# Optimization experiments

Measured on AMD Instinct MI355X. Metric: run time of the kernel, lower is better.

Reference implementation:

```python
import jax, jax.numpy as jnp
import numpy as np

B, D, H, E = 1024, 64, 128, 8192


def setup_inputs() -> dict:
    key = jax.random.key(0)
    ks = jax.random.split(key, 10)
    def w(k, shape, fan_in):
        return jax.random.normal(k, shape, jnp.float32) / np.float32(np.sqrt(fan_in))
    return {
        "mu": jax.random.normal(ks[0], (B, D), jnp.float32),
        "current_edge_index": jax.random.randint(ks[1], (2, E), 0, B),
        "W1": w(ks[2], (D, H), D),   "b1": jnp.zeros((H,), jnp.float32),
        "W2": w(ks[3], (H, H), H),   "b2": jnp.zeros((H,), jnp.float32),
        "Ws1": w(ks[4], (2 * H, H), 2 * H), "bs1": jnp.zeros((H,), jnp.float32),
        "Ws2": w(ks[5], (H, 1), H),  "bs2": jnp.zeros((1,), jnp.float32),
        "Wg1": w(ks[6], (2 * H, H), 2 * H), "bg1": jnp.zeros((H,), jnp.float32),
        "Wg2": w(ks[7], (H, D), H), "bg2": jnp.zeros((D,), jnp.float32),
    }


def _gcn(x, W, b, src, dst, n):
    loop = jnp.arange(n)
    s = jnp.concatenate([src, loop])
    d = jnp.concatenate([dst, loop])
    deg = jax.ops.segment_sum(jnp.ones_like(s, x.dtype), d, num_segments=n)
    dinv = jax.lax.rsqrt(jnp.maximum(deg, 1e-12))
    norm = dinv[s] * dinv[d]                      # [E+n]
    xw = x @ W                                    # [n,H]
    out = jax.ops.segment_sum(xw[s] * norm[:, None], d, num_segments=n)
    return out + b


def _pairwise_scores(h, Ws1, bs1, Ws2, bs2):
    # score_mlp([h_i || h_j]) for all pairs, vectorized: split first-layer weight
    A = h @ Ws1[:H]                               # [B,H] contribution of h_i
    C = h @ Ws1[H:]                               # [B,H] contribution of h_j
    pre = jax.nn.relu(A[:, None, :] + C[None, :, :] + bs1)   # [B,B,H]
    s = (pre @ Ws2)[..., 0] + bs2[0]              # [B,B]
    up = jnp.triu(s, 1)                           # only i<j computed in original
    return up + up.T                              # symmetric, zero diagonal


def _kruskal(scores_np, n):
    iu, ju = np.triu_indices(n, 1)
    w = scores_np[iu, ju]
    order = np.argsort(-w, kind="stable")         # descending, stable like list.sort
    parent = list(range(n))
    rank = [0] * n
    def find(u):
        while parent[u] != u:
            parent[u] = parent[parent[u]]
            u = parent[u]
        return u
    edges = []
    for k in order:
        i, j = int(iu[k]), int(ju[k])
        ri, rj = find(i), find(j)
        if ri == rj:
            continue
        if rank[ri] < rank[rj]:
            parent[ri] = rj
        elif rank[ri] > rank[rj]:
            parent[rj] = ri
        else:
            parent[rj] = ri
            rank[ri] += 1
        edges.append((i, j))
        if len(edges) == n - 1:
            break
    return np.asarray(edges, dtype=np.int64)      # [n-1, 2]


def reference(mu, current_edge_index, W1, b1, W2, b2, Ws1, bs1, Ws2, bs2, Wg1, bg1, Wg2, bg2):
    src, dst = current_edge_index[0], current_edge_index[1]
    h = jax.nn.relu(_gcn(mu, W1, b1, src, dst, B))
    h = jax.nn.relu(_gcn(h, W2, b2, src, dst, B))
    scores = _pairwise_scores(h, Ws1, bs1, Ws2, bs2)          # [B,B]
    mst = _kruskal(np.asarray(scores), B)                     # [B-1,2], i<j
    ei = jnp.asarray(mst[:, 0])
    ej = jnp.asarray(mst[:, 1])
    # bidirectional edge index: src=[i,j,...], dst=[j,i,...]
    new_edge_index = jnp.stack([
        jnp.stack([ei, ej], axis=1).reshape(-1),
        jnp.stack([ej, ei], axis=1).reshape(-1),
    ], axis=0)                                                # [2, 2*(B-1)]
    hp = jnp.concatenate([h[ei], h[ej]], axis=1)              # [B-1, 2H]
    gamma = jnp.tanh(jax.nn.relu(hp @ Wg1 + bg1) @ Wg2 + bg2) # [B-1, D]
    return (new_edge_index, gamma)
```

## Files before the change

kernel.cpp:

```cpp
#include <hip/hip_runtime.h>
#include <hip/hip_bf16.h>
#include <math.h>

#define BN 1024
#define DIN 64
#define HD 128
#define EN 8192
#define SLOTS_STRIDE 64
#define MMR 8
#define NC 128

typedef unsigned long long u64;

__global__ void k_fill(const int* dst, int* cnt, int* slots) {
    int e = blockIdx.x * blockDim.x + threadIdx.x;
    if (e < EN) {
        int d = dst[e];
        int p = atomicAdd(&cnt[d], 1);
        if (p < SLOTS_STRIDE) slots[d * SLOTS_STRIDE + p] = e;
    }
}

__global__ __launch_bounds__(128) void k_finish(int* slots, const int* cnt, float* dinv) {
    __shared__ int buf[128][65];
    int tid = threadIdx.x;
    int t = blockIdx.x * 128 + tid;
    int n = cnt[t];
    if (n > SLOTS_STRIDE) n = SLOTS_STRIDE;
    for (int k = 0; k < n; k++) buf[tid][k] = slots[t * SLOTS_STRIDE + k];
    for (int k = 1; k < n; k++) {
        int v = buf[tid][k];
        int q = k - 1;
        while (q >= 0 && buf[tid][q] > v) { buf[tid][q + 1] = buf[tid][q]; q--; }
        buf[tid][q + 1] = v;
    }
    for (int k = 0; k < n; k++) slots[t * SLOTS_STRIDE + k] = buf[tid][k];
    dinv[t] = 1.0f / sqrtf(fmaxf((float)(n + 1), 1e-12f));
}

__global__ __launch_bounds__(128) void k_mm8(const float* x, const float* W, const float* bias,
                                             float* out, int K) {
    __shared__ float xr[MMR][HD];
    int col = threadIdx.x;
    int r0 = blockIdx.x * MMR;
#pragma unroll
    for (int r = 0; r < MMR; r++)
        if (col < K) xr[r][col] = x[(r0 + r) * K + col];
    __syncthreads();
    float b = bias ? bias[col] : 0.0f;
    float acc[MMR];
#pragma unroll
    for (int r = 0; r < MMR; r++) acc[r] = b;
#pragma unroll 4
    for (int k = 0; k < K; k++) {
        float w = W[k * HD + col];
#pragma unroll
        for (int r = 0; r < MMR; r++) acc[r] = fmaf(xr[r][k], w, acc[r]);
    }
#pragma unroll
    for (int r = 0; r < MMR; r++) out[(r0 + r) * HD + col] = acc[r];
}

__global__ __launch_bounds__(128) void k_mmAC(const float* h, const float* Ws1, const float* bs1,
                                              float* Aa, float* Cc) {
    __shared__ float xr[MMR][HD];
    int col = threadIdx.x;
    int r0 = blockIdx.x * MMR;
#pragma unroll
    for (int r = 0; r < MMR; r++) xr[r][col] = h[(r0 + r) * HD + col];
    __syncthreads();
    float accA[MMR], accC[MMR];
    float bc = bs1[col];
#pragma unroll
    for (int r = 0; r < MMR; r++) { accA[r] = 0.0f; accC[r] = bc; }
#pragma unroll 2
    for (int k = 0; k < HD; k++) {
        float wa = Ws1[k * HD + col];
        float wc = Ws1[(HD + k) * HD + col];
#pragma unroll
        for (int r = 0; r < MMR; r++) {
            accA[r] = fmaf(xr[r][k], wa, accA[r]);
            accC[r] = fmaf(xr[r][k], wc, accC[r]);
        }
    }
#pragma unroll
    for (int r = 0; r < MMR; r++) {
        Aa[(r0 + r) * HD + col] = accA[r];
        Cc[(r0 + r) * HD + col] = accC[r];
    }
}

__global__ __launch_bounds__(128) void k_gather(const float* xw, const float* bvec, const int* src,
                                                const int* slots, const int* cnt,
                                                const float* dinv, float* hout) {
    int d = blockIdx.x, t = threadIdx.x;
    float dd = dinv[d];
    float acc = 0.0f;
    int base = d * SLOTS_STRIDE, n = cnt[d];
    if (n > SLOTS_STRIDE) n = SLOTS_STRIDE;
    for (int s = 0; s < n; s++) {
        int e = slots[base + s];
        int sn = src[e];
        acc = fmaf(xw[sn * HD + t], dinv[sn] * dd, acc);
    }
    acc = fmaf(xw[d * HD + t], dd * dd, acc);
    acc += bvec[t];
    hout[d * HD + t] = fmaxf(acc, 0.0f);
}

__device__ __forceinline__ u64 edge_key(float w, int i, int j) {
    unsigned u = __float_as_uint(w);
    u = (u & 0x80000000u) ? ~u : (u | 0x80000000u);
    int a = i < j ? i : j, b = i < j ? j : i;
    unsigned packed = (unsigned)(a * BN + b);
    return ((u64)u << 20) | (u64)(0xFFFFFu - packed);
}

__global__ __launch_bounds__(256) void k_scores(const float* Aa, const float* Cc,
                                                const float* Ws2, const float* bs2v,
                                                float* S, u64* best) {
    int bi = blockIdx.y, bj = blockIdx.x;
    if (bi > bj) return;
    __shared__ float As[64][68];
    __shared__ float Cs[64][68];
    __shared__ float w2[HD];
    __shared__ u64 rmax[64], cmax[64];
    int tid = threadIdx.x;
    int R = bi * 64, Cb = bj * 64;
    if (tid < HD) w2[tid] = Ws2[tid];
    if (tid < 64) { rmax[tid] = 0ull; cmax[tid] = 0ull; }
    int tx = tid & 15, ty = tid >> 4;
    float acc[4][4] = {};
    for (int half = 0; half < 2; half++) {
        int k0 = half * 64;
        __syncthreads();
        for (int idx = tid; idx < 64 * 64; idx += 256) {
            int row = idx >> 6;
            int kk = idx & 63;
            As[kk][row] = Aa[(R + row) * HD + k0 + kk];
            Cs[kk][row] = Cc[(Cb + row) * HD + k0 + kk];
        }
        __syncthreads();
        for (int kk = 0; kk < 64; kk++) {
            float4 av = *(const float4*)&As[kk][ty * 4];
            float4 cv = *(const float4*)&Cs[kk][tx * 4];
            float wk = w2[k0 + kk];
            float ar[4] = {av.x, av.y, av.z, av.w};
            float cr[4] = {cv.x, cv.y, cv.z, cv.w};
#pragma unroll
            for (int r = 0; r < 4; r++)
#pragma unroll
                for (int q = 0; q < 4; q++) {
                    float tv = fmaxf(ar[r] + cr[q], 0.0f);
                    acc[r][q] = fmaf(tv, wk, acc[r][q]);
                }
        }
    }
    float b2 = bs2v[0];
    u64 rloc[4] = {0ull, 0ull, 0ull, 0ull};
    u64 cloc[4] = {0ull, 0ull, 0ull, 0ull};
#pragma unroll
    for (int r = 0; r < 4; r++)
#pragma unroll
        for (int q = 0; q < 4; q++) {
            int gr = R + ty * 4 + r, gc = Cb + tx * 4 + q;
            float v = acc[r][q] + b2;
            if (gr < gc) {
                S[gr * BN + gc] = v;
                S[gc * BN + gr] = v;
                u64 key = edge_key(v, gr, gc);
                if (key > rloc[r]) rloc[r] = key;
                if (key > cloc[q]) cloc[q] = key;
            } else if (gr == gc) S[gr * BN + gc] = 0.0f;
        }
#pragma unroll
    for (int r = 0; r < 4; r++) {
        if (rloc[r]) atomicMax(&rmax[ty * 4 + r], rloc[r]);
        if (cloc[r]) atomicMax(&cmax[tx * 4 + r], cloc[r]);
    }
    __syncthreads();
    if (tid < 64) {
        if (rmax[tid]) atomicMax(&best[R + tid], rmax[tid]);
    } else if (tid < 128) {
        if (cmax[tid - 64]) atomicMax(&best[Cb + tid - 64], cmax[tid - 64]);
    }
}

__global__ __launch_bounds__(256) void k_best(const float* S, const int* comp,
                                              u64* best, const int* mstcnt) {
    if (*mstcnt >= BN - 1) return;
    int lane = threadIdx.x & 63;
    int i = blockIdx.x * 4 + (threadIdx.x >> 6);
    int ci = comp[i];
    const float* Srow = S + (size_t)i * BN;
    u64 loc = 0ull;
    for (int j = lane; j < BN; j += 64)
        if (comp[j] != ci) {
            u64 key = edge_key(Srow[j], i, j);
            if (key > loc) loc = key;
        }
#pragma unroll
    for (int off = 32; off > 0; off >>= 1) {
        u64 o = __shfl_xor(loc, off);
        if (o > loc) loc = o;
    }
    if (lane == 0 && loc) atomicMax(&best[ci], loc);
}

__global__ __launch_bounds__(1024) void k_merge1(u64* best, int* comp, u64* mst, int* mstcnt) {
    __shared__ int pa[BN], pb[BN];
    int c = threadIdx.x;
    u64 e = best[c];
    unsigned packed = 0xFFFFFu - (unsigned)(e & 0xFFFFFu);
    int a = packed >> 10, b = packed & 1023;
    int t = (a == c) ? b : a;
    pa[c] = t;
    __syncthreads();
    bool mutual = (pa[t] == c);
    int p0 = pa[c];
    if (mutual && c < t) p0 = c;
    __syncthreads();
    pa[c] = p0;
    __syncthreads();
    if (!(mutual && c > t)) {
        int idx = atomicAdd(mstcnt, 1);
        mst[idx] = e;
    }
    for (int it = 0; it < 10; it++) {
        pb[c] = pa[pa[c]];
        __syncthreads();
        pa[c] = pb[c];
        __syncthreads();
    }
    comp[c] = pa[c];
    best[c] = 0ull;
}

__global__ __launch_bounds__(1024) void k_merge(int* comp, u64* best, u64* mst, int* mstcnt,
                                                int* compD, int* ncompG, int emitDense) {
    __shared__ int pa[BN], pb[BN];
    int c = threadIdx.x;
    if (*mstcnt >= BN - 1) return;
    int myComp = comp[c];
    bool root = (myComp == c);
    u64 e = best[c];
    int t = c;
    if (root && e) {
        unsigned packed = 0xFFFFFu - (unsigned)(e & 0xFFFFFu);
        int a = packed >> 10, b = packed & 1023;
        int ca = comp[a], cb = comp[b];
        t = (ca == c) ? cb : ca;
    }
    pa[c] = (root && e) ? t : c;
    __syncthreads();
    bool mutual = root && e && (pa[t] == c);
    int p0 = pa[c];
    if (mutual && c < t) p0 = c;
    __syncthreads();
    pa[c] = p0;
    __syncthreads();
    if (root && e && !(mutual && c > t)) {
        int idx = atomicAdd(mstcnt, 1);
        mst[idx] = e;
    }
    for (int it = 0; it < 10; it++) {
        pb[c] = pa[pa[c]];
        __syncthreads();
        pa[c] = pb[c];
        __syncthreads();
    }
    comp[c] = pa[myComp];
    best[c] = 0ull;
    if (!emitDense) return;
    __syncthreads();
    int isR = (comp[c] == c) ? 1 : 0;
    pa[c] = isR;
    __syncthreads();
    for (int d = 1; d < BN; d <<= 1) {
        int v = (c >= d) ? pa[c - d] : 0;
        __syncthreads();
        pa[c] += v;
        __syncthreads();
    }
    if (isR) pb[c] = pa[c] - 1;
    __syncthreads();
    compD[c] = pb[comp[c]];
    if (c == BN - 1) *ncompG = pa[BN - 1];
}

__global__ __launch_bounds__(256) void k_Gsp(const float* S, const int* compD,
                                             const int* mstcnt, u64* spG) {
    if (*mstcnt >= BN - 1) return;
    __shared__ u64 t[NC];
    int tid = threadIdx.x;
    int i = blockIdx.x;
    int ci = compD[i];
    if (tid < NC) t[tid] = 0ull;
    __syncthreads();
    const float* Srow = S + (size_t)i * BN;
    for (int j = tid; j < BN; j += 256) {
        int cj = compD[j];
        if (j != i && cj != ci) atomicMax(&t[cj], edge_key(Srow[j], i, j));
    }
    __syncthreads();
    if (tid < NC && t[tid]) atomicMax(&spG[(size_t)ci * NC + tid], t[tid]);
}

struct FinSm {
    union {
        u64 sp[NC][NC];
        u64 sk[BN];
    } u;
    int cnd[BN];
    int ccomp[NC], cpa[NC], cpb[NC];
    u64 cbest[NC];
    int lcnt;
};

__global__ __launch_bounds__(1024) void k_mstfin(const u64* spG, const int* compD,
                                                 const int* ncompG, const int* mstcntG,
                                                 u64* mstG, float* out, int* pairs) {
    __shared__ FinSm sm;
    int c = threadIdx.x;
    int total = *mstcntG;
    if (total < BN - 1) {
        int nc = *ncompG;
        for (int idx = c; idx < NC * NC; idx += 1024) ((u64*)sm.u.sp)[idx] = spG[idx];
        sm.cnd[c] = compD[c];
        if (c < NC) { sm.ccomp[c] = c; sm.cbest[c] = 0ull; }
        if (c == 0) sm.lcnt = 0;
        __syncthreads();
        for (int rr = 0; rr < 8 && total < BN - 1; rr++) {
            if (c < nc) {
                int g = sm.ccomp[c];
                u64 m = 0ull;
                for (int c2 = 0; c2 < nc; c2++)
                    if (sm.ccomp[c2] != g) {
                        u64 v = sm.u.sp[c][c2];
                        if (v > m) m = v;
                    }
                if (m) atomicMax(&sm.cbest[g], m);
            }
            __syncthreads();
            if (c < nc) {
                bool root = (sm.ccomp[c] == c);
                u64 e = sm.cbest[c];
                int t2 = c;
                if (root && e) {
                    unsigned packed = 0xFFFFFu - (unsigned)(e & 0xFFFFFu);
                    int a = packed >> 10, b = packed & 1023;
                    int ga = sm.ccomp[sm.cnd[a]], gb = sm.ccomp[sm.cnd[b]];
                    t2 = (ga == c) ? gb : ga;
                }
                sm.cpa[c] = (root && e) ? t2 : c;
            }
            __syncthreads();
            if (c < nc) {
                bool root = (sm.ccomp[c] == c);
                u64 e = sm.cbest[c];
                int t2 = sm.cpa[c];
                bool mutual = root && e && (sm.cpa[t2] == c);
                int p0 = sm.cpa[c];
                if (mutual && c < t2) p0 = c;
                sm.cpb[c] = p0;
                if (root && e && !(mutual && c > t2)) {
                    int idx = total + atomicAdd(&sm.lcnt, 1);
                    mstG[idx] = e;
                }
            }
            __syncthreads();
            if (c < nc) sm.cpa[c] = sm.cpb[c];
            __syncthreads();
            for (int it = 0; it < 7; it++) {
                if (c < nc) sm.cpb[c] = sm.cpa[sm.cpa[c]];
                __syncthreads();
                if (c < nc) sm.cpa[c] = sm.cpb[c];
                __syncthreads();
            }
            if (c < nc) {
                sm.ccomp[c] = sm.cpa[sm.ccomp[c]];
                sm.cbest[c] = 0ull;
            }
            __syncthreads();
            int added = sm.lcnt;
            __syncthreads();
            total += added;
            if (c == 0) sm.lcnt = 0;
            __syncthreads();
        }
    }
    __syncthreads();
    sm.u.sk[c] = (c < BN - 1) ? mstG[c] : 0ull;
    __syncthreads();
    if (c < BN - 1) {
        u64 mykey = sm.u.sk[c];
        int rk = 0;
        for (int f = 0; f < BN - 1; f++) rk += (sm.u.sk[f] > mykey) ? 1 : 0;
        unsigned packed = 0xFFFFFu - (unsigned)(mykey & 0xFFFFFu);
        int i = packed >> 10, j2 = packed & 1023;
        out[2 * rk] = (float)i;
        out[2 * rk + 1] = (float)j2;
        out[2046 + 2 * rk] = (float)j2;
        out[2046 + 2 * rk + 1] = (float)i;
        pairs[2 * rk] = i;
        pairs[2 * rk + 1] = j2;
    }
}

__global__ __launch_bounds__(128) void k_gamma(const float* h, const int* pairs,
                                               const float* Wg1, const float* bg1,
                                               const float* Wg2, const float* bg2, float* out) {
    int eidx = blockIdx.x;
    __shared__ float hp[2 * HD];
    __shared__ float z1[HD];
    int t = threadIdx.x;
    int i = pairs[2 * eidx], j = pairs[2 * eidx + 1];
    hp[t] = h[i * HD + t];
    hp[HD + t] = h[j * HD + t];
    __syncthreads();
    float acc = bg1[t];
    for (int k = 0; k < 2 * HD; k++) acc = fmaf(hp[k], Wg1[k * HD + t], acc);
    z1[t] = fmaxf(acc, 0.0f);
    __syncthreads();
    if (t < DIN) {
        float g = bg2[t];
        for (int k = 0; k < HD; k++) g = fmaf(z1[k], Wg2[k * DIN + t], g);
        out[4092 + eidx * DIN + t] = tanhf(g);
    }
}

extern "C" void kernel_launch(void* const* d_in, const int* in_sizes, int n_in,
                              void* d_out, int out_size, void* d_ws, size_t ws_size,
                              hipStream_t stream) {
    const float* mu  = (const float*)d_in[0];
    const int*   ei  = (const int*)d_in[1];
    const float* W1  = (const float*)d_in[2];
    const float* b1  = (const float*)d_in[3];
    const float* W2  = (const float*)d_in[4];
    const float* b2  = (const float*)d_in[5];
    const float* Ws1 = (const float*)d_in[6];
    const float* bs1 = (const float*)d_in[7];
    const float* Ws2 = (const float*)d_in[8];
    const float* bs2 = (const float*)d_in[9];
    const float* Wg1 = (const float*)d_in[10];
    const float* bg1 = (const float*)d_in[11];
    const float* Wg2 = (const float*)d_in[12];
    const float* bg2 = (const float*)d_in[13];
    float* out = (float*)d_out;

    const int* src = ei;
    const int* dst = ei + EN;

    char* ws = (char*)d_ws;
    int*   slots = (int*)(ws);
    float* S     = (float*)(ws);
    float* xw    = (float*)(ws + 4194304);
    float* h1    = (float*)(ws + 4718592);
    float* h2    = (float*)(ws + 5242880);
    float* Aa    = (float*)(ws + 5767168);
    float* Cc    = (float*)(ws + 6291456);
    int*   cnt   = (int*)(ws + 6815744);
    u64*   best  = (u64*)(ws + 6819840);
    int*   mstcnt = (int*)(ws + 6828032);
    u64*   spG   = (u64*)(ws + 6832128);
    int*   comp  = (int*)(ws + 6963200);
    u64*   mstG  = (u64*)(ws + 6967296);
    int*   pairs = (int*)(ws + 6975488);
    int*   compD = (int*)(ws + 6983680);
    int*   ncomp = (int*)(ws + 6987776);
    float* dinv  = (float*)(ws + 6991872);

    hipMemsetAsync(ws + 6815744, 0, 147456, stream);

    k_fill<<<EN / 256, 256, 0, stream>>>(dst, cnt, slots);
    k_finish<<<BN / 128, 128, 0, stream>>>(slots, cnt, dinv);

    k_mm8<<<BN / MMR, HD, 0, stream>>>(mu, W1, nullptr, xw, DIN);
    k_gather<<<BN, HD, 0, stream>>>(xw, b1, src, slots, cnt, dinv, h1);
    k_mm8<<<BN / MMR, HD, 0, stream>>>(h1, W2, nullptr, xw, HD);
    k_gather<<<BN, HD, 0, stream>>>(xw, b2, src, slots, cnt, dinv, h2);

    k_mmAC<<<BN / MMR, HD, 0, stream>>>(h2, Ws1, bs1, Aa, Cc);

    k_scores<<<dim3(16, 16), 256, 0, stream>>>(Aa, Cc, Ws2, bs2, S, best);

    k_merge1<<<1, 1024, 0, stream>>>(best, comp, mstG, mstcnt);
    k_best<<<BN / 4, 256, 0, stream>>>(S, comp, best, mstcnt);
    k_merge<<<1, 1024, 0, stream>>>(comp, best, mstG, mstcnt, compD, ncomp, 0);
    k_best<<<BN / 4, 256, 0, stream>>>(S, comp, best, mstcnt);
    k_merge<<<1, 1024, 0, stream>>>(comp, best, mstG, mstcnt, compD, ncomp, 1);

    k_Gsp<<<BN, 256, 0, stream>>>(S, compD, mstcnt, spG);
    k_mstfin<<<1, 1024, 0, stream>>>(spG, compD, ncomp, mstcnt, mstG, out, pairs);

    k_gamma<<<BN - 1, HD, 0, stream>>>(h2, pairs, Wg1, bg1, Wg2, bg2, out);
}
```

Before: 162.9 us.

## Retune matmul kernels, batch gamma MLP, compact score grid, skip extra Boruvka round

The small matmul kernels now handle 4 rows per 256-thread block instead of 8 rows per 128 threads, which doubles the block count. The gather kernel stages neighbour indices and weights in shared memory. The score kernel launches only the 136 upper-triangle tiles rather than 256 blocks with early exits. The gamma MLP processes 8 edges per block so each weight load is reused across edges. The second Boruvka round can now be skipped once the component count is small enough, with the first merge emitting dense component ids. These are several separate changes, and the conditional skip relies on ncomp being valid after the first merge.

```diff
diff --git a/kernel.cpp b/kernel.cpp
--- a/kernel.cpp
+++ b/kernel.cpp
@@ -7,7 +7,8 @@
 #define HD 128
 #define EN 8192
 #define SLOTS_STRIDE 64
-#define MMR 8
+#define MMR4 4
+#define EGR 8
 #define NC 128
 
 typedef unsigned long long u64;
@@ -38,71 +39,72 @@
     dinv[t] = 1.0f / sqrtf(fmaxf((float)(n + 1), 1e-12f));
 }
 
-__global__ __launch_bounds__(128) void k_mm8(const float* x, const float* W, const float* bias,
+__global__ __launch_bounds__(256) void k_mm4(const float* x, const float* W, const float* bias,
                                              float* out, int K) {
-    __shared__ float xr[MMR][HD];
-    int col = threadIdx.x;
-    int r0 = blockIdx.x * MMR;
-#pragma unroll
-    for (int r = 0; r < MMR; r++)
-        if (col < K) xr[r][col] = x[(r0 + r) * K + col];
-    __syncthreads();
+    __shared__ float xr[MMR4][HD];
+    int tid = threadIdx.x;
+    int r0 = blockIdx.x * MMR4;
+    for (int idx = tid; idx < MMR4 * K; idx += 256)
+        xr[idx / K][idx % K] = x[r0 * K + idx];
+    __syncthreads();
+    int col = tid & 127, half = tid >> 7;
     float b = bias ? bias[col] : 0.0f;
-    float acc[MMR];
-#pragma unroll
-    for (int r = 0; r < MMR; r++) acc[r] = b;
+    float a0 = b, a1 = b;
 #pragma unroll 4
     for (int k = 0; k < K; k++) {
         float w = W[k * HD + col];
-#pragma unroll
-        for (int r = 0; r < MMR; r++) acc[r] = fmaf(xr[r][k], w, acc[r]);
-    }
-#pragma unroll
-    for (int r = 0; r < MMR; r++) out[(r0 + r) * HD + col] = acc[r];
-}
-
-__global__ __launch_bounds__(128) void k_mmAC(const float* h, const float* Ws1, const float* bs1,
+        a0 = fmaf(xr[half * 2 + 0][k], w, a0);
+        a1 = fmaf(xr[half * 2 + 1][k], w, a1);
+    }
+    out[(r0 + half * 2 + 0) * HD + col] = a0;
+    out[(r0 + half * 2 + 1) * HD + col] = a1;
+}
+
+__global__ __launch_bounds__(256) void k_mmAC(const float* h, const float* Ws1, const float* bs1,
                                               float* Aa, float* Cc) {
-    __shared__ float xr[MMR][HD];
-    int col = threadIdx.x;
-    int r0 = blockIdx.x * MMR;
-#pragma unroll
-    for (int r = 0; r < MMR; r++) xr[r][col] = h[(r0 + r) * HD + col];
-    __syncthreads();
-    float accA[MMR], accC[MMR];
+    __shared__ float xr[MMR4][HD];
+    int tid = threadIdx.x;
+    int r0 = blockIdx.x * MMR4;
+    for (int idx = tid; idx < MMR4 * HD; idx += 256)
+        xr[idx >> 7][idx & 127] = h[r0 * HD + idx];
+    __syncthreads();
+    int col = tid & 127, half = tid >> 7;
     float bc = bs1[col];
-#pragma unroll
-    for (int r = 0; r < MMR; r++) { accA[r] = 0.0f; accC[r] = bc; }
+    float A0 = 0.0f, A1 = 0.0f, C0 = bc, C1 = bc;
 #pragma unroll 2
     for (int k = 0; k < HD; k++) {
         float wa = Ws1[k * HD + col];
         float wc = Ws1[(HD + k) * HD + col];
-#pragma unroll
-        for (int r = 0; r < MMR; r++) {
-            accA[r] = fmaf(xr[r][k], wa, accA[r]);
-            accC[r] = fmaf(xr[r][k], wc, accC[r]);
-        }
-    }
-#pragma unroll
-    for (int r = 0; r < MMR; r++) {
-        Aa[(r0 + r) * HD + col] = accA[r];
-        Cc[(r0 + r) * HD + col] = accC[r];
-    }
+        A0 = fmaf(xr[half * 2 + 0][k], wa, A0);
+        A1 = fmaf(xr[half * 2 + 1][k], wa, A1);
+        C0 = fmaf(xr[half * 2 + 0][k], wc, C0);
+        C1 = fmaf(xr[half * 2 + 1][k], wc, C1);
+    }
+    Aa[(r0 + half * 2 + 0) * HD + col] = A0;
+    Aa[(r0 + half * 2 + 1) * HD + col] = A1;
+    Cc[(r0 + half * 2 + 0) * HD + col] = C0;
+    Cc[(r0 + half * 2 + 1) * HD + col] = C1;
 }
 
 __global__ __launch_bounds__(128) void k_gather(const float* xw, const float* bvec, const int* src,
                                                 const int* slots, const int* cnt,
                                                 const float* dinv, float* hout) {
+    __shared__ int sn_s[SLOTS_STRIDE];
+    __shared__ float w_s[SLOTS_STRIDE];
     int d = blockIdx.x, t = threadIdx.x;
     float dd = dinv[d];
+    int n = cnt[d];
+    if (n > SLOTS_STRIDE) n = SLOTS_STRIDE;
+    if (t < n) {
+        int e = slots[d * SLOTS_STRIDE + t];
+        int sn = src[e];
+        sn_s[t] = sn;
+        w_s[t] = dinv[sn] * dd;
+    }
+    __syncthreads();
     float acc = 0.0f;
-    int base = d * SLOTS_STRIDE, n = cnt[d];
-    if (n > SLOTS_STRIDE) n = SLOTS_STRIDE;
-    for (int s = 0; s < n; s++) {
-        int e = slots[base + s];
-        int sn = src[e];
-        acc = fmaf(xw[sn * HD + t], dinv[sn] * dd, acc);
-    }
+    for (int s = 0; s < n; s++)
+        acc = fmaf(xw[sn_s[s] * HD + t], w_s[s], acc);
     acc = fmaf(xw[d * HD + t], dd * dd, acc);
     acc += bvec[t];
     hout[d * HD + t] = fmaxf(acc, 0.0f);
@@ -119,8 +121,10 @@
 __global__ __launch_bounds__(256) void k_scores(const float* Aa, const float* Cc,
                                                 const float* Ws2, const float* bs2v,
                                                 float* S, u64* best) {
-    int bi = blockIdx.y, bj = blockIdx.x;
-    if (bi > bj) return;
+    int bid = blockIdx.x;
+    int bi = 0, rem = bid;
+    while (rem >= 16 - bi) { rem -= 16 - bi; bi++; }
+    int bj = bi + rem;
     __shared__ float As[64][68];
     __shared__ float Cs[64][68];
     __shared__ float w2[HD];
@@ -187,8 +191,10 @@
 }
 
 __global__ __launch_bounds__(256) void k_best(const float* S, const int* comp,
-                                              u64* best, const int* mstcnt) {
+                                              u64* best, const int* mstcnt,
+                                              const int* ncompG, int ncGuard) {
     if (*mstcnt >= BN - 1) return;
+    if (ncGuard && *ncompG <= NC) return;
     int lane = threadIdx.x & 63;
     int i = blockIdx.x * 4 + (threadIdx.x >> 6);
     int ci = comp[i];
@@ -237,10 +243,12 @@
 }
 
 __global__ __launch_bounds__(1024) void k_merge(int* comp, u64* best, u64* mst, int* mstcnt,
-                                                int* compD, int* ncompG, int emitDense) {
+                                                int* compD, int* ncompG, int emitDense,
+                                                int ncGuard) {
     __shared__ int pa[BN], pb[BN];
     int c = threadIdx.x;
     if (*mstcnt >= BN - 1) return;
+    if (ncGuard && *ncompG <= NC) return;
     int myComp = comp[c];
     bool root = (myComp == c);
     u64 e = best[c];
@@ -407,25 +415,52 @@
     }
 }
 
-__global__ __launch_bounds__(128) void k_gamma(const float* h, const int* pairs,
-                                               const float* Wg1, const float* bg1,
-                                               const float* Wg2, const float* bg2, float* out) {
-    int eidx = blockIdx.x;
-    __shared__ float hp[2 * HD];
-    __shared__ float z1[HD];
-    int t = threadIdx.x;
-    int i = pairs[2 * eidx], j = pairs[2 * eidx + 1];
-    hp[t] = h[i * HD + t];
-    hp[HD + t] = h[j * HD + t];
-    __syncthreads();
-    float acc = bg1[t];
-    for (int k = 0; k < 2 * HD; k++) acc = fmaf(hp[k], Wg1[k * HD + t], acc);
-    z1[t] = fmaxf(acc, 0.0f);
-    __syncthreads();
-    if (t < DIN) {
-        float g = bg2[t];
-        for (int k = 0; k < HD; k++) g = fmaf(z1[k], Wg2[k * DIN + t], g);
-        out[4092 + eidx * DIN + t] = tanhf(g);
+__global__ __launch_bounds__(256) void k_gamma8(const float* h, const int* pairs,
+                                                const float* Wg1, const float* bg1,
+                                                const float* Wg2, const float* bg2, float* out) {
+    __shared__ float hp[EGR][2 * HD];
+    __shared__ float z1[EGR][HD];
+    int tid = threadIdx.x;
+    int e0 = blockIdx.x * EGR;
+    for (int idx = tid; idx < EGR * 2 * HD; idx += 256) {
+        int eo = idx >> 8;
+        int k = idx & 255;
+        int e = e0 + eo;
+        if (e < BN - 1) {
+            int node = (k < HD) ? pairs[2 * e] : pairs[2 * e + 1];
+            hp[eo][k] = h[node * HD + (k & 127)];
+        }
+    }
+    __syncthreads();
+    {
+        int c = tid & 127, eg = tid >> 7;
+        float b = bg1[c];
+        float a0 = b, a1 = b, a2 = b, a3 = b;
+        for (int k = 0; k < 2 * HD; k++) {
+            float w = Wg1[k * HD + c];
+            a0 = fmaf(hp[eg * 4 + 0][k], w, a0);
+            a1 = fmaf(hp[eg * 4 + 1][k], w, a1);
+            a2 = fmaf(hp[eg * 4 + 2][k], w, a2);
+            a3 = fmaf(hp[eg * 4 + 3][k], w, a3);
+        }
+        z1[eg * 4 + 0][c] = fmaxf(a0, 0.0f);
+        z1[eg * 4 + 1][c] = fmaxf(a1, 0.0f);
+        z1[eg * 4 + 2][c] = fmaxf(a2, 0.0f);
+        z1[eg * 4 + 3][c] = fmaxf(a3, 0.0f);
+    }
+    __syncthreads();
+    {
+        int co = tid & 63, eh = tid >> 6;
+        float b = bg2[co];
+        float g0 = b, g1 = b;
+        for (int k = 0; k < HD; k++) {
+            float w = Wg2[k * DIN + co];
+            g0 = fmaf(z1[eh * 2 + 0][k], w, g0);
+            g1 = fmaf(z1[eh * 2 + 1][k], w, g1);
+        }
+        int ea = e0 + eh * 2, eb = ea + 1;
+        if (ea < BN - 1) out[4092 + ea * DIN + co] = tanhf(g0);
+        if (eb < BN - 1) out[4092 + eb * DIN + co] = tanhf(g1);
     }
 }
 
@@ -475,23 +510,23 @@
     k_fill<<<EN / 256, 256, 0, stream>>>(dst, cnt, slots);
     k_finish<<<BN / 128, 128, 0, stream>>>(slots, cnt, dinv);
 
-    k_mm8<<<BN / MMR, HD, 0, stream>>>(mu, W1, nullptr, xw, DIN);
+    k_mm4<<<BN / MMR4, 256, 0, stream>>>(mu, W1, nullptr, xw, DIN);
     k_gather<<<BN, HD, 0, stream>>>(xw, b1, src, slots, cnt, dinv, h1);
-    k_mm8<<<BN / MMR, HD, 0, stream>>>(h1, W2, nullptr, xw, HD);
+    k_mm4<<<BN / MMR4, 256, 0, stream>>>(h1, W2, nullptr, xw, HD);
     k_gather<<<BN, HD, 0, stream>>>(xw, b2, src, slots, cnt, dinv, h2);
 
-    k_mmAC<<<BN / MMR, HD, 0, stream>>>(h2, Ws1, bs1, Aa, Cc);
-
-    k_scores<<<dim3(16, 16), 256, 0, stream>>>(Aa, Cc, Ws2, bs2, S, best);
+    k_mmAC<<<BN / MMR4, 256, 0, stream>>>(h2, Ws1, bs1, Aa, Cc);
+
+    k_scores<<<136, 256, 0, stream>>>(Aa, Cc, Ws2, bs2, S, best);
 
     k_merge1<<<1, 1024, 0, stream>>>(best, comp, mstG, mstcnt);
-    k_best<<<BN / 4, 256, 0, stream>>>(S, comp, best, mstcnt);
-    k_merge<<<1, 1024, 0, stream>>>(comp, best, mstG, mstcnt, compD, ncomp, 0);
-    k_best<<<BN / 4, 256, 0, stream>>>(S, comp, best, mstcnt);
-    k_merge<<<1, 1024, 0, stream>>>(comp, best, mstG, mstcnt, compD, ncomp, 1);
+    k_best<<<BN / 4, 256, 0, stream>>>(S, comp, best, mstcnt, ncomp, 0);
+    k_merge<<<1, 1024, 0, stream>>>(comp, best, mstG, mstcnt, compD, ncomp, 1, 0);
+    k_best<<<BN / 4, 256, 0, stream>>>(S, comp, best, mstcnt, ncomp, 1);
+    k_merge<<<1, 1024, 0, stream>>>(comp, best, mstG, mstcnt, compD, ncomp, 1, 1);
 
     k_Gsp<<<BN, 256, 0, stream>>>(S, compD, mstcnt, spG);
     k_mstfin<<<1, 1024, 0, stream>>>(spG, compD, ncomp, mstcnt, mstG, out, pairs);
 
-    k_gamma<<<BN - 1, HD, 0, stream>>>(h2, pairs, Wg1, bg1, Wg2, bg2, out);
-}
+    k_gamma8<<<(BN - 1 + EGR - 1) / EGR, 256, 0, stream>>>(h2, pairs, Wg1, bg1, Wg2, bg2, out);
+}
```

After: 164.5 us. About the same (+1.0%).
